# Performance work log

Hardware: AMD Instinct MI355X
Metric: run time of the kernel (lower is better)

The kernel has to match this reference:

```python
import jax, jax.numpy as jnp
import numpy as np

N_NODES = 100000
N_EDGES = 1600000
IN_DIM = 256
OUT_DIM = 128
SELF_LOOP_W = 2.0  # improved=True


def setup_inputs() -> dict:
    key = jax.random.key(0)
    ks = jax.random.split(key, 9)
    x = jax.random.normal(ks[0], (N_NODES, IN_DIM), dtype=jnp.float32)
    edge_index = jax.random.randint(ks[1], (2, N_EDGES), 0, N_NODES, dtype=jnp.int64)
    edge_weight = jax.random.uniform(ks[2], (N_EDGES,), dtype=jnp.float32)
    s1 = 1.0 / np.sqrt(IN_DIM)
    s2 = 1.0 / np.sqrt(OUT_DIM)
    W1 = jax.random.normal(ks[3], (IN_DIM, OUT_DIM), dtype=jnp.float32) * s1
    b1 = jnp.zeros((OUT_DIM,), dtype=jnp.float32)
    W_mu = jax.random.normal(ks[4], (OUT_DIM, OUT_DIM), dtype=jnp.float32) * s2
    b_mu = jnp.zeros((OUT_DIM,), dtype=jnp.float32)
    W_var = jax.random.normal(ks[5], (OUT_DIM, OUT_DIM), dtype=jnp.float32) * s2
    b_var = jnp.zeros((OUT_DIM,), dtype=jnp.float32)
    return {"x": x, "edge_index": edge_index, "edge_weight": edge_weight,
            "W1": W1, "b1": b1, "W_mu": W_mu, "b_mu": b_mu,
            "W_var": W_var, "b_var": b_var}


def _gcn_norm(edge_index, edge_weight, num_nodes):
    # add self loops with fill value 2.0 (improved=True), then symmetric norm
    loop = jnp.arange(num_nodes, dtype=edge_index.dtype)
    row = jnp.concatenate([edge_index[0], loop])
    col = jnp.concatenate([edge_index[1], loop])
    ew = jnp.concatenate([edge_weight,
                          jnp.full((num_nodes,), SELF_LOOP_W, dtype=edge_weight.dtype)])
    deg = jax.ops.segment_sum(ew, col, num_segments=num_nodes)
    dis = jnp.where(deg > 0, jax.lax.rsqrt(jnp.where(deg > 0, deg, 1.0)), 0.0)
    norm = dis[row] * ew * dis[col]
    return row, col, norm


def _gcn_conv(x, row, col, norm, W, b, num_nodes):
    xw = x @ W                      # [N, out]
    msg = xw[row] * norm[:, None]   # [E+N, out] per-edge messages
    out = jax.ops.segment_sum(msg, col, num_segments=num_nodes)
    return out + b


def reference(x, edge_index, edge_weight, W1, b1, W_mu, b_mu, W_var, b_var):
    n = x.shape[0]
    row, col, norm = _gcn_norm(edge_index, edge_weight, n)
    feat = jax.nn.relu(_gcn_conv(x, row, col, norm, W1, b1, n))
    mu = _gcn_conv(feat, row, col, norm, W_mu, b_mu, n)
    var = _gcn_conv(feat, row, col, norm, W_var, b_var, n)
    return (mu, var)
```

## Files before the change

kernel.cpp:

```cpp
#include <hip/hip_runtime.h>
#include <hip/hip_bf16.h>

#define CDIV(a,b) (((a)+(b)-1)/(b))

typedef __attribute__((ext_vector_type(8))) short short8;
typedef __attribute__((ext_vector_type(4))) float f32x4;

static __device__ inline short f2bf(float f) {
    union { __hip_bfloat16 h; short s; } u;
    u.h = __float2bfloat16(f);
    return u.s;
}
static __device__ inline ushort f2bfu(float f) { return (ushort)f2bf(f); }
static __device__ inline float bfu_lo(uint v) { return __uint_as_float(v << 16); }
static __device__ inline float bfu_hi(uint v) { return __uint_as_float(v & 0xffff0000u); }


__global__ __launch_bounds__(512) void k_init(const float* __restrict__ W1,
                                              short* __restrict__ W1t,
                                              const float* __restrict__ Wmu,
                                              const float* __restrict__ Wvar,
                                              short* __restrict__ Wcat) {
    int i = blockIdx.x * 512 + threadIdx.x;
    if (i < 128 * 256) {
        int k = i % 256, col = i / 256;
        W1t[i] = f2bf(W1[(size_t)k * 128 + col]);
    } else if (i < 2 * 128 * 256) {
        int j = i - 128 * 256;
        int k = j & 127, col = j >> 7;
        float v = (col < 128) ? Wmu[(size_t)k * 128 + col] : Wvar[(size_t)k * 128 + (col - 128)];
        Wcat[j] = f2bf(v);
    }
}


__global__ __launch_bounds__(512) void k_bhist(const int* __restrict__ coli,
                                               int* __restrict__ bhist,
                                               int E, int chunk, int nbk) {
    __shared__ int h[256];
    int b = blockIdx.x, t = threadIdx.x, nblk = gridDim.x;
    for (int i = t; i < nbk; i += 512) h[i] = 0;
    __syncthreads();
    int e0 = b * chunk, e1 = min(E, e0 + chunk);
    for (int e = e0 + t; e < e1; e += 512)
        atomicAdd(&h[coli[e] >> 9], 1);
    __syncthreads();
    for (int i = t; i < nbk; i += 512)
        bhist[i * nblk + b] = h[i];
}

__global__ __launch_bounds__(256) void kscanA(const int* __restrict__ in,
                                              int* __restrict__ out,
                                              int* __restrict__ part, int n) {
    int t = threadIdx.x;
    int base = blockIdx.x * 1024 + t * 4;
    int v0 = (base + 0 < n) ? in[base + 0] : 0;
    int v1 = (base + 1 < n) ? in[base + 1] : 0;
    int v2 = (base + 2 < n) ? in[base + 2] : 0;
    int v3 = (base + 3 < n) ? in[base + 3] : 0;
    int tsum = v0 + v1 + v2 + v3;
    int lane = t & 63, wv = t >> 6;
    int val = tsum;
    #pragma unroll
    for (int d = 1; d < 64; d <<= 1) {
        int u = __shfl_up(val, d, 64);
        if (lane >= d) val += u;
    }
    __shared__ int ws[4];
    if (lane == 63) ws[wv] = val;
    __syncthreads();
    int woff = 0;
    #pragma unroll
    for (int i = 0; i < 4; ++i) if (i < wv) woff += ws[i];
    int excl = woff + val - tsum;
    if (base + 0 < n) out[base + 0] = excl;  excl += v0;
    if (base + 1 < n) out[base + 1] = excl;  excl += v1;
    if (base + 2 < n) out[base + 2] = excl;  excl += v2;
    if (base + 3 < n) out[base + 3] = excl;
    if (t == 255) part[blockIdx.x] = woff + val;
}

__global__ __launch_bounds__(128) void kscanB(int* part, int nb, int* tailp, int tailv) {
    int t = threadIdx.x;
    int v = (t < nb) ? part[t] : 0;
    int lane = t & 63, wv = t >> 6;
    int val = v;
    #pragma unroll
    for (int d = 1; d < 64; d <<= 1) {
        int u = __shfl_up(val, d, 64);
        if (lane >= d) val += u;
    }
    __shared__ int ws[2];
    if (lane == 63) ws[wv] = val;
    __syncthreads();
    int woff = (wv == 1) ? ws[0] : 0;
    if (t < nb) part[t] = woff + val - v;
    if (t == 0 && tailp) *tailp = tailv;
}

__global__ __launch_bounds__(256) void kscanC(int* __restrict__ out,
                                              const int* __restrict__ part, int n) {
    int i = blockIdx.x * 256 + threadIdx.x;
    if (i < n) out[i] += part[i >> 10];
}

__global__ __launch_bounds__(512) void k_bucket(const int* __restrict__ rowi,
                                                const int* __restrict__ coli,
                                                const float* __restrict__ ew,
                                                const int* __restrict__ excl,
                                                int* __restrict__ bcol,
                                                int2* __restrict__ bre,
                                                int E, int chunk, int nbk) {
    __shared__ int cur[256];
    int b = blockIdx.x, t = threadIdx.x, nblk = gridDim.x;
    for (int i = t; i < nbk; i += 512) cur[i] = 0;
    __syncthreads();
    int e0 = b * chunk, e1 = min(E, e0 + chunk);
    for (int e = e0 + t; e < e1; e += 512) {
        int c = coli[e];
        int bk = c >> 9;
        int pos = excl[bk * nblk + b] + atomicAdd(&cur[bk], 1);
        bcol[pos] = c;
        bre[pos]  = make_int2(rowi[e], __float_as_int(ew[e]));
    }
}

__global__ __launch_bounds__(512) void k_fine(const int* __restrict__ bcol,
                                              const int2* __restrict__ bre,
                                              const int* __restrict__ excl,
                                              int* __restrict__ rank,
                                              int* __restrict__ gcnt,
                                              int* __restrict__ gews,
                                              int E, int nblk, int n) {
    __shared__ int cnt[512], ews[512];
    int bk = blockIdx.x, t = threadIdx.x;
    cnt[t] = 0; ews[t] = 0;
    __syncthreads();
    int s0 = excl[bk * nblk];
    int s1 = (bk + 1 < gridDim.x) ? excl[(bk + 1) * nblk] : E;
    for (int p = s0 + t; p < s1; p += 512) {
        int cl = bcol[p] & 511;
        rank[p] = atomicAdd(&cnt[cl], 1);
        int q = (int)(__int_as_float(bre[p].y) * 16777216.0f + 0.5f);
        atomicAdd(&ews[cl], q);
    }
    __syncthreads();
    int c = bk * 512 + t;
    if (c < n) { gcnt[c] = cnt[t]; gews[c] = ews[t]; }
}

__global__ __launch_bounds__(256) void k_dis(const int* __restrict__ gews,
                                             float* __restrict__ dis, int n) {
    int i = blockIdx.x * 256 + threadIdx.x;
    if (i < n)
        dis[i] = rsqrtf(2.0f + (float)gews[i] * (1.0f / 16777216.0f));
}

__global__ __launch_bounds__(512) void k_place(const int* __restrict__ bcol,
                                               const int2* __restrict__ bre,
                                               const int* __restrict__ rank,
                                               const int* __restrict__ row_ptr,
                                               const float* __restrict__ dis,
                                               int2* __restrict__ csr, int E) {
    int p = blockIdx.x * 512 + threadIdx.x;
    if (p < E) {
        int c = bcol[p];
        int2 re = bre[p];
        csr[row_ptr[c] + rank[p]] =
            make_int2(re.x, __float_as_int(dis[re.x] * __int_as_float(re.y)));
    }
}


__global__ __launch_bounds__(512) void k_gemm1(const float* __restrict__ A,
                                               const short* __restrict__ Bt,
                                               ushort* __restrict__ C, int n) {
    const int K = 256, KH = 128;
    __shared__ short Blds[128 * KH];
    int t = threadIdx.x;

    int wave = t >> 6, lane = t & 63;
    int lg = lane >> 4, lr = lane & 15;
    long row_base = (long)blockIdx.x * 256 + wave * 32;

    long ra0 = row_base + lr;      if (ra0 > n - 1) ra0 = n - 1;
    long ra1 = row_base + 16 + lr; if (ra1 > n - 1) ra1 = n - 1;

    f32x4 acc[2][8];
    #pragma unroll
    for (int i = 0; i < 2; ++i)
        #pragma unroll
        for (int j = 0; j < 8; ++j) acc[i][j] = (f32x4){0.f, 0.f, 0.f, 0.f};

    const float* pa0 = A + ra0 * K + lg * 8;
    const float* pa1 = A + ra1 * K + lg * 8;

    #pragma unroll
    for (int p = 0; p < 2; ++p) {
        if (p) __syncthreads();
        const int CHK = KH / 8;
        for (int c = t; c < 128 * CHK; c += 512) {
            int colw = c / CHK;
            int kb  = (c % CHK) * 16;
            int dst = colw * (KH * 2) + (kb ^ ((colw & 7) << 4));
            *(float4*)((char*)Blds + dst) =
                *(const float4*)((const char*)Bt + (size_t)colw * (K * 2) + p * (KH * 2) + kb);
        }
        __syncthreads();

        for (int k0 = 0; k0 < KH; k0 += 32) {
            int kg = p * KH + k0;
            float4 x0 = *(const float4*)(pa0 + kg);
            float4 x1 = *(const float4*)(pa0 + kg + 4);
            float4 y0 = *(const float4*)(pa1 + kg);
            float4 y1 = *(const float4*)(pa1 + kg + 4);
            short8 a0, a1;
            a0[0]=f2bf(x0.x); a0[1]=f2bf(x0.y); a0[2]=f2bf(x0.z); a0[3]=f2bf(x0.w);
            a0[4]=f2bf(x1.x); a0[5]=f2bf(x1.y); a0[6]=f2bf(x1.z); a0[7]=f2bf(x1.w);
            a1[0]=f2bf(y0.x); a1[1]=f2bf(y0.y); a1[2]=f2bf(y0.z); a1[3]=f2bf(y0.w);
            a1[4]=f2bf(y1.x); a1[5]=f2bf(y1.y); a1[6]=f2bf(y1.z); a1[7]=f2bf(y1.w);

            int kb = (k0 + lg * 8) * 2;
            #pragma unroll
            for (int cb = 0; cb < 8; ++cb) {
                int colm = cb * 16 + lr;
                short8 bfr = *(short8*)((char*)Blds + colm * (KH * 2) + (kb ^ ((colm & 7) << 4)));
                acc[0][cb] = __builtin_amdgcn_mfma_f32_16x16x32_bf16(a0, bfr, acc[0][cb], 0, 0, 0);
                acc[1][cb] = __builtin_amdgcn_mfma_f32_16x16x32_bf16(a1, bfr, acc[1][cb], 0, 0, 0);
            }
        }
    }

    #pragma unroll
    for (int rf = 0; rf < 2; ++rf) {
        #pragma unroll
        for (int cb = 0; cb < 8; ++cb) {
            int colm = cb * 16 + lr;
            #pragma unroll
            for (int r = 0; r < 4; ++r) {
                long row = row_base + rf * 16 + lg * 4 + r;
                if (row < n) C[row * 128 + colm] = f2bfu(acc[rf][cb][r]);
            }
        }
    }
}


template<int OUTMODE>
__global__ __launch_bounds__(256) void k_agg(const uint2* __restrict__ src,
                                             const int* __restrict__ row_ptr,
                                             const int2* __restrict__ csr,
                                             const float* __restrict__ dis,
                                             const float* __restrict__ bias,
                                             uint2* __restrict__ dst, int n) {
    int wid = (blockIdx.x * 256 + threadIdx.x) >> 6;
    int lane = threadIdx.x & 63;
    int hb = lane >> 5, lc = lane & 31;
    if (wid >= n) return;
    int e0 = row_ptr[wid], e1 = row_ptr[wid + 1];

    float p00=0.f,p01=0.f,p02=0.f,p03=0.f;
    float p10=0.f,p11=0.f,p12=0.f,p13=0.f;
    float p20=0.f,p21=0.f,p22=0.f,p23=0.f;
    float p30=0.f,p31=0.f,p32=0.f,p33=0.f;

    int e = e0;
    for (; e + 7 < e1; e += 8) {
        int2 c0 = csr[e     + hb];
        int2 c1 = csr[e + 2 + hb];
        int2 c2 = csr[e + 4 + hb];
        int2 c3 = csr[e + 6 + hb];
        uint2 v0 = src[(size_t)c0.x * 32 + lc];
        uint2 v1 = src[(size_t)c1.x * 32 + lc];
        uint2 v2 = src[(size_t)c2.x * 32 + lc];
        uint2 v3 = src[(size_t)c3.x * 32 + lc];
        float w0 = __int_as_float(c0.y), w1 = __int_as_float(c1.y);
        float w2 = __int_as_float(c2.y), w3 = __int_as_float(c3.y);
        p00 += w0 * bfu_lo(v0.x); p01 += w0 * bfu_hi(v0.x);
        p02 += w0 * bfu_lo(v0.y); p03 += w0 * bfu_hi(v0.y);
        p10 += w1 * bfu_lo(v1.x); p11 += w1 * bfu_hi(v1.x);
        p12 += w1 * bfu_lo(v1.y); p13 += w1 * bfu_hi(v1.y);
        p20 += w2 * bfu_lo(v2.x); p21 += w2 * bfu_hi(v2.x);
        p22 += w2 * bfu_lo(v2.y); p23 += w2 * bfu_hi(v2.y);
        p30 += w3 * bfu_lo(v3.x); p31 += w3 * bfu_hi(v3.x);
        p32 += w3 * bfu_lo(v3.y); p33 += w3 * bfu_hi(v3.y);
    }
    for (; e + 1 < e1; e += 2) {
        int2 c = csr[e + hb];
        uint2 v = src[(size_t)c.x * 32 + lc];
        float w = __int_as_float(c.y);
        p00 += w * bfu_lo(v.x); p01 += w * bfu_hi(v.x);
        p02 += w * bfu_lo(v.y); p03 += w * bfu_hi(v.y);
    }
    if (e < e1 && hb == 0) {
        int2 c = csr[e];
        uint2 v = src[(size_t)c.x * 32 + lc];
        float w = __int_as_float(c.y);
        p10 += w * bfu_lo(v.x); p11 += w * bfu_hi(v.x);
        p12 += w * bfu_lo(v.y); p13 += w * bfu_hi(v.y);
    }

    float x0 = (p00 + p10) + (p20 + p30);
    float x1 = (p01 + p11) + (p21 + p31);
    float x2 = (p02 + p12) + (p22 + p32);
    float x3 = (p03 + p13) + (p23 + p33);
    x0 = x0 + __shfl_xor(x0, 32);
    x1 = x1 + __shfl_xor(x1, 32);
    x2 = x2 + __shfl_xor(x2, 32);
    x3 = x3 + __shfl_xor(x3, 32);

    float dc = dis[wid];
    uint2 sv = src[(size_t)wid * 32 + lc];
    float sw = 2.f * dc * dc;
    float o0 = dc * x0 + sw * bfu_lo(sv.x);
    float o1 = dc * x1 + sw * bfu_hi(sv.x);
    float o2 = dc * x2 + sw * bfu_lo(sv.y);
    float o3 = dc * x3 + sw * bfu_hi(sv.y);
    if constexpr (OUTMODE == 0) {
        float4 bv = *(const float4*)(bias + lc * 4);
        o0 += bv.x; o1 += bv.y; o2 += bv.z; o3 += bv.w;
        o0 = fmaxf(o0, 0.f); o1 = fmaxf(o1, 0.f);
        o2 = fmaxf(o2, 0.f); o3 = fmaxf(o3, 0.f);
    }
    if (hb == 0)
        dst[(size_t)wid * 32 + lc] =
            make_uint2((uint)f2bfu(o0) | ((uint)f2bfu(o1) << 16),
                       (uint)f2bfu(o2) | ((uint)f2bfu(o3) << 16));
}


__global__ __launch_bounds__(512) void k_gemm2(const short* __restrict__ A,
                                               const short* __restrict__ Bt,
                                               const float* __restrict__ bmu,
                                               const float* __restrict__ bvar,
                                               float* __restrict__ out,
                                               int n) {
    const int K = 128;
    __shared__ short Blds[256 * K];
    int t = threadIdx.x;

    const int CHK = K / 8;
    for (int c = t; c < 256 * CHK; c += 512) {
        int col = c / CHK;
        int kb  = (c % CHK) * 16;
        int dst = col * (K * 2) + (kb ^ ((col & 7) << 4));
        *(float4*)((char*)Blds + dst) =
            *(const float4*)((const char*)Bt + (size_t)col * (K * 2) + kb);
    }
    __syncthreads();

    int wave = t >> 6, lane = t & 63;
    int lg = lane >> 4, lr = lane & 15;
    int colbase = (wave & 1) * 128;
    long row_base = (long)blockIdx.x * 128 + (wave >> 1) * 32;

    long ra0 = row_base + lr;      if (ra0 > n - 1) ra0 = n - 1;
    long ra1 = row_base + 16 + lr; if (ra1 > n - 1) ra1 = n - 1;

    f32x4 acc[2][8];
    #pragma unroll
    for (int i = 0; i < 2; ++i)
        #pragma unroll
        for (int j = 0; j < 8; ++j) acc[i][j] = (f32x4){0.f, 0.f, 0.f, 0.f};

    const short* pa0 = A + ra0 * K + lg * 8;
    const short* pa1 = A + ra1 * K + lg * 8;

    #pragma unroll
    for (int k0 = 0; k0 < K; k0 += 32) {
        short8 a0 = *(const short8*)(pa0 + k0);
        short8 a1 = *(const short8*)(pa1 + k0);
        int kb = (k0 + lg * 8) * 2;
        #pragma unroll
        for (int cb = 0; cb < 8; ++cb) {
            int col = colbase + cb * 16 + lr;
            short8 b = *(short8*)((char*)Blds + col * (K * 2) + (kb ^ ((col & 7) << 4)));
            acc[0][cb] = __builtin_amdgcn_mfma_f32_16x16x32_bf16(a0, b, acc[0][cb], 0, 0, 0);
            acc[1][cb] = __builtin_amdgcn_mfma_f32_16x16x32_bf16(a1, b, acc[1][cb], 0, 0, 0);
        }
    }

    #pragma unroll
    for (int rf = 0; rf < 2; ++rf) {
        #pragma unroll
        for (int cb = 0; cb < 8; ++cb) {
            int colc = colbase + cb * 16 + lr;
            bool is_var = colc >= 128;
            int col = is_var ? colc - 128 : colc;
            float bv = is_var ? bvar[col] : bmu[col];
            size_t obase = is_var ? (size_t)n * 128 : 0;
            #pragma unroll
            for (int r = 0; r < 4; ++r) {
                long row = row_base + rf * 16 + lg * 4 + r;
                if (row < n)
                    __builtin_nontemporal_store(acc[rf][cb][r] + bv,
                                                &out[obase + (size_t)row * 128 + col]);
            }
        }
    }
}


extern "C" void kernel_launch(void* const* d_in, const int* in_sizes, int n_in,
                              void* d_out, int out_size, void* d_ws, size_t ws_size,
                              hipStream_t stream) {
    const float* x    = (const float*)d_in[0];
    const int*   ei   = (const int*)d_in[1];
    const float* ew   = (const float*)d_in[2];
    const float* W1   = (const float*)d_in[3];
    const float* b1   = (const float*)d_in[4];
    const float* Wmu  = (const float*)d_in[5];
    const float* bmu  = (const float*)d_in[6];
    const float* Wvar = (const float*)d_in[7];
    const float* bvar = (const float*)d_in[8];

    const int E = in_sizes[2];
    const int N = in_sizes[0] / 256;
    const int* rowi = ei;
    const int* coli = ei + E;

    char* base = (char*)d_ws;
    size_t off = 0;
    auto alloc = [&](size_t bytes) -> void* {
        void* p = base + off;
        off = (off + bytes + 511) & ~(size_t)511;
        return p;
    };
    const int NBLK = 256;
    const int nbk  = CDIV(N, 512);
    const int chunk = CDIV(E, NBLK);
    const int nh   = nbk * NBLK;

    int*   bhist   = (int*)  alloc((size_t)nh * 4);
    int*   excl    = (int*)  alloc((size_t)nh * 4);
    int*   part    = (int*)  alloc(256 * 4);
    int*   bcol    = (int*)  alloc((size_t)E * 4);
    int2*  bre     = (int2*) alloc((size_t)E * 8);
    int*   rank    = (int*)  alloc((size_t)E * 4);
    int*   gcnt    = (int*)  alloc((size_t)N * 4);
    int*   gews    = (int*)  alloc((size_t)N * 4);
    int*   row_ptr = (int*)  alloc((size_t)(N + 1) * 4);
    float* dis     = (float*)alloc((size_t)N * 4);
    int2*  csr     = (int2*) alloc((size_t)E * 8);
    uint*  xw      = (uint*) alloc((size_t)N * 64 * 4);
    uint*  feat    = (uint*) alloc((size_t)N * 64 * 4);
    short* W1t     = (short*)alloc((size_t)256 * 128 * 2);
    short* Wcat    = (short*)alloc((size_t)256 * 128 * 2);
    uint*  g       = xw;

    k_init<<<CDIV(2 * 128 * 256, 512), 512, 0, stream>>>(W1, W1t, Wmu, Wvar, Wcat);

    k_gemm1<<<CDIV(N, 256), 512, 0, stream>>>(x, W1t, (ushort*)xw, N);

    k_bhist<<<NBLK, 512, 0, stream>>>(coli, bhist, E, chunk, nbk);
    kscanA<<<CDIV(nh, 1024), 256, 0, stream>>>(bhist, excl, part, nh);
    kscanB<<<1, 128, 0, stream>>>(part, CDIV(nh, 1024), nullptr, 0);
    kscanC<<<CDIV(nh, 256), 256, 0, stream>>>(excl, part, nh);
    k_bucket<<<NBLK, 512, 0, stream>>>(rowi, coli, ew, excl, bcol, bre, E, chunk, nbk);
    k_fine<<<nbk, 512, 0, stream>>>(bcol, bre, excl, rank, gcnt, gews, E, NBLK, N);
    kscanA<<<CDIV(N, 1024), 256, 0, stream>>>(gcnt, row_ptr, part, N);
    kscanB<<<1, 128, 0, stream>>>(part, CDIV(N, 1024), &row_ptr[N], E);
    kscanC<<<CDIV(N, 256), 256, 0, stream>>>(row_ptr, part, N);
    k_dis<<<CDIV(N, 256), 256, 0, stream>>>(gews, dis, N);
    k_place<<<CDIV(E, 512), 512, 0, stream>>>(bcol, bre, rank, row_ptr, dis, csr, E);

    k_agg<0><<<CDIV(N * 64, 256), 256, 0, stream>>>((const uint2*)xw, row_ptr, csr, dis, b1, (uint2*)feat, N);
    k_agg<1><<<CDIV(N * 64, 256), 256, 0, stream>>>((const uint2*)feat, row_ptr, csr, dis, nullptr, (uint2*)g, N);
    k_gemm2<<<CDIV(N, 128), 512, 0, stream>>>((const short*)g, Wcat, bmu, bvar, (float*)d_out, N);
}
```

Measured before the change: 286.6 us.

## Fuse CSR build: per-bucket local scan, packed bucket records, bucket-wise placement

```diff
diff --git a/kernel.cpp b/kernel.cpp
--- a/kernel.cpp
+++ b/kernel.cpp
@@ -80,7 +80,7 @@
     if (t == 255) part[blockIdx.x] = woff + val;
 }
 
-__global__ __launch_bounds__(128) void kscanB(int* part, int nb, int* tailp, int tailv) {
+__global__ __launch_bounds__(128) void kscanB(int* part, int nb) {
     int t = threadIdx.x;
     int v = (t < nb) ? part[t] : 0;
     int lane = t & 63, wv = t >> 6;
@@ -95,7 +95,6 @@
     __syncthreads();
     int woff = (wv == 1) ? ws[0] : 0;
     if (t < nb) part[t] = woff + val - v;
-    if (t == 0 && tailp) *tailp = tailv;
 }
 
 __global__ __launch_bounds__(256) void kscanC(int* __restrict__ out,
@@ -108,8 +107,8 @@
                                                 const int* __restrict__ coli,
                                                 const float* __restrict__ ew,
                                                 const int* __restrict__ excl,
-                                                int* __restrict__ bcol,
-                                                int2* __restrict__ bre,
+                                                int* __restrict__ bx,
+                                                int* __restrict__ bw,
                                                 int E, int chunk, int nbk) {
     __shared__ int cur[256];
     int b = blockIdx.x, t = threadIdx.x, nblk = gridDim.x;
@@ -120,18 +119,17 @@
         int c = coli[e];
         int bk = c >> 9;
         int pos = excl[bk * nblk + b] + atomicAdd(&cur[bk], 1);
-        bcol[pos] = c;
-        bre[pos]  = make_int2(rowi[e], __float_as_int(ew[e]));
-    }
-}
-
-__global__ __launch_bounds__(512) void k_fine(const int* __restrict__ bcol,
-                                              const int2* __restrict__ bre,
-                                              const int* __restrict__ excl,
-                                              int* __restrict__ rank,
-                                              int* __restrict__ gcnt,
-                                              int* __restrict__ gews,
-                                              int E, int nblk, int n) {
+        bx[pos] = ((c & 511) << 17) | rowi[e];
+        bw[pos] = __float_as_int(ew[e]);
+    }
+}
+
+__global__ __launch_bounds__(512) void k_fine2(const int* __restrict__ bx,
+                                               const int* __restrict__ bw,
+                                               const int* __restrict__ excl,
+                                               int* __restrict__ row_ptr,
+                                               float* __restrict__ dis,
+                                               int E, int nblk, int n) {
     __shared__ int cnt[512], ews[512];
     int bk = blockIdx.x, t = threadIdx.x;
     cnt[t] = 0; ews[t] = 0;
@@ -139,35 +137,54 @@
     int s0 = excl[bk * nblk];
     int s1 = (bk + 1 < gridDim.x) ? excl[(bk + 1) * nblk] : E;
     for (int p = s0 + t; p < s1; p += 512) {
-        int cl = bcol[p] & 511;
-        rank[p] = atomicAdd(&cnt[cl], 1);
-        int q = (int)(__int_as_float(bre[p].y) * 16777216.0f + 0.5f);
+        int cl = bx[p] >> 17;
+        atomicAdd(&cnt[cl], 1);
+        int q = (int)(__int_as_float(bw[p]) * 16777216.0f + 0.5f);
         atomicAdd(&ews[cl], q);
     }
     __syncthreads();
+    int v = cnt[t];
+    int lane = t & 63, wv = t >> 6;
+    int val = v;
+    #pragma unroll
+    for (int d = 1; d < 64; d <<= 1) {
+        int u = __shfl_up(val, d, 64);
+        if (lane >= d) val += u;
+    }
+    __shared__ int ws2[8];
+    if (lane == 63) ws2[wv] = val;
+    __syncthreads();
+    int woff = 0;
+    #pragma unroll
+    for (int i = 0; i < 8; ++i) if (i < wv) woff += ws2[i];
+    int lexcl = woff + val - v;
     int c = bk * 512 + t;
-    if (c < n) { gcnt[c] = cnt[t]; gews[c] = ews[t]; }
-}
-
-__global__ __launch_bounds__(256) void k_dis(const int* __restrict__ gews,
-                                             float* __restrict__ dis, int n) {
-    int i = blockIdx.x * 256 + threadIdx.x;
-    if (i < n)
-        dis[i] = rsqrtf(2.0f + (float)gews[i] * (1.0f / 16777216.0f));
-}
-
-__global__ __launch_bounds__(512) void k_place(const int* __restrict__ bcol,
-                                               const int2* __restrict__ bre,
-                                               const int* __restrict__ rank,
+    if (c < n) {
+        row_ptr[c] = s0 + lexcl;
+        dis[c] = rsqrtf(2.0f + (float)ews[t] * (1.0f / 16777216.0f));
+    }
+    if (bk == 0 && t == 0) row_ptr[n] = E;
+}
+
+__global__ __launch_bounds__(512) void k_place(const int* __restrict__ bx,
+                                               const int* __restrict__ bw,
+                                               const int* __restrict__ excl,
                                                const int* __restrict__ row_ptr,
                                                const float* __restrict__ dis,
-                                               int2* __restrict__ csr, int E) {
-    int p = blockIdx.x * 512 + threadIdx.x;
-    if (p < E) {
-        int c = bcol[p];
-        int2 re = bre[p];
-        csr[row_ptr[c] + rank[p]] =
-            make_int2(re.x, __float_as_int(dis[re.x] * __int_as_float(re.y)));
+                                               int2* __restrict__ csr,
+                                               int E, int nblk, int n) {
+    __shared__ int cur[512];
+    int bk = blockIdx.x, t = threadIdx.x;
+    cur[t] = 0;
+    __syncthreads();
+    int s0 = excl[bk * nblk];
+    int s1 = (bk + 1 < gridDim.x) ? excl[(bk + 1) * nblk] : E;
+    int cbase = bk * 512;
+    for (int p = s0 + t; p < s1; p += 512) {
+        int u = bx[p];
+        int cl = u >> 17, r = u & 0x1FFFF;
+        int pos = row_ptr[cbase + cl] + atomicAdd(&cur[cl], 1);
+        csr[pos] = make_int2(r, __float_as_int(dis[r] * __int_as_float(bw[p])));
     }
 }
 
@@ -265,11 +282,43 @@
     float p30=0.f,p31=0.f,p32=0.f,p33=0.f;
 
     int e = e0;
+    for (; e + 15 < e1; e += 16) {
+        int2 c0 = csr[e      + hb], c1 = csr[e + 2  + hb];
+        int2 c2 = csr[e + 4  + hb], c3 = csr[e + 6  + hb];
+        int2 c4 = csr[e + 8  + hb], c5 = csr[e + 10 + hb];
+        int2 c6 = csr[e + 12 + hb], c7 = csr[e + 14 + hb];
+        uint2 v0 = src[(size_t)c0.x * 32 + lc];
+        uint2 v1 = src[(size_t)c1.x * 32 + lc];
+        uint2 v2 = src[(size_t)c2.x * 32 + lc];
+        uint2 v3 = src[(size_t)c3.x * 32 + lc];
+        uint2 v4 = src[(size_t)c4.x * 32 + lc];
+        uint2 v5 = src[(size_t)c5.x * 32 + lc];
+        uint2 v6 = src[(size_t)c6.x * 32 + lc];
+        uint2 v7 = src[(size_t)c7.x * 32 + lc];
+        float w0 = __int_as_float(c0.y), w1 = __int_as_float(c1.y);
+        float w2 = __int_as_float(c2.y), w3 = __int_as_float(c3.y);
+        float w4 = __int_as_float(c4.y), w5 = __int_as_float(c5.y);
+        float w6 = __int_as_float(c6.y), w7 = __int_as_float(c7.y);
+        p00 += w0 * bfu_lo(v0.x); p01 += w0 * bfu_hi(v0.x);
+        p02 += w0 * bfu_lo(v0.y); p03 += w0 * bfu_hi(v0.y);
+        p10 += w1 * bfu_lo(v1.x); p11 += w1 * bfu_hi(v1.x);
+        p12 += w1 * bfu_lo(v1.y); p13 += w1 * bfu_hi(v1.y);
+        p20 += w2 * bfu_lo(v2.x); p21 += w2 * bfu_hi(v2.x);
+        p22 += w2 * bfu_lo(v2.y); p23 += w2 * bfu_hi(v2.y);
+        p30 += w3 * bfu_lo(v3.x); p31 += w3 * bfu_hi(v3.x);
+        p32 += w3 * bfu_lo(v3.y); p33 += w3 * bfu_hi(v3.y);
+        p00 += w4 * bfu_lo(v4.x); p01 += w4 * bfu_hi(v4.x);
+        p02 += w4 * bfu_lo(v4.y); p03 += w4 * bfu_hi(v4.y);
+        p10 += w5 * bfu_lo(v5.x); p11 += w5 * bfu_hi(v5.x);
+        p12 += w5 * bfu_lo(v5.y); p13 += w5 * bfu_hi(v5.y);
+        p20 += w6 * bfu_lo(v6.x); p21 += w6 * bfu_hi(v6.x);
+        p22 += w6 * bfu_lo(v6.y); p23 += w6 * bfu_hi(v6.y);
+        p30 += w7 * bfu_lo(v7.x); p31 += w7 * bfu_hi(v7.x);
+        p32 += w7 * bfu_lo(v7.y); p33 += w7 * bfu_hi(v7.y);
+    }
     for (; e + 7 < e1; e += 8) {
-        int2 c0 = csr[e     + hb];
-        int2 c1 = csr[e + 2 + hb];
-        int2 c2 = csr[e + 4 + hb];
-        int2 c3 = csr[e + 6 + hb];
+        int2 c0 = csr[e + hb],     c1 = csr[e + 2 + hb];
+        int2 c2 = csr[e + 4 + hb], c3 = csr[e + 6 + hb];
         uint2 v0 = src[(size_t)c0.x * 32 + lc];
         uint2 v1 = src[(size_t)c1.x * 32 + lc];
         uint2 v2 = src[(size_t)c2.x * 32 + lc];
@@ -434,11 +483,8 @@
     int*   bhist   = (int*)  alloc((size_t)nh * 4);
     int*   excl    = (int*)  alloc((size_t)nh * 4);
     int*   part    = (int*)  alloc(256 * 4);
-    int*   bcol    = (int*)  alloc((size_t)E * 4);
-    int2*  bre     = (int2*) alloc((size_t)E * 8);
-    int*   rank    = (int*)  alloc((size_t)E * 4);
-    int*   gcnt    = (int*)  alloc((size_t)N * 4);
-    int*   gews    = (int*)  alloc((size_t)N * 4);
+    int*   bx      = (int*)  alloc((size_t)E * 4);
+    int*   bw      = (int*)  alloc((size_t)E * 4);
     int*   row_ptr = (int*)  alloc((size_t)(N + 1) * 4);
     float* dis     = (float*)alloc((size_t)N * 4);
     int2*  csr     = (int2*) alloc((size_t)E * 8);
@@ -449,20 +495,15 @@
     uint*  g       = xw;
 
     k_init<<<CDIV(2 * 128 * 256, 512), 512, 0, stream>>>(W1, W1t, Wmu, Wvar, Wcat);
-
     k_gemm1<<<CDIV(N, 256), 512, 0, stream>>>(x, W1t, (ushort*)xw, N);
 
     k_bhist<<<NBLK, 512, 0, stream>>>(coli, bhist, E, chunk, nbk);
     kscanA<<<CDIV(nh, 1024), 256, 0, stream>>>(bhist, excl, part, nh);
-    kscanB<<<1, 128, 0, stream>>>(part, CDIV(nh, 1024), nullptr, 0);
+    kscanB<<<1, 128, 0, stream>>>(part, CDIV(nh, 1024));
     kscanC<<<CDIV(nh, 256), 256, 0, stream>>>(excl, part, nh);
-    k_bucket<<<NBLK, 512, 0, stream>>>(rowi, coli, ew, excl, bcol, bre, E, chunk, nbk);
-    k_fine<<<nbk, 512, 0, stream>>>(bcol, bre, excl, rank, gcnt, gews, E, NBLK, N);
-    kscanA<<<CDIV(N, 1024), 256, 0, stream>>>(gcnt, row_ptr, part, N);
-    kscanB<<<1, 128, 0, stream>>>(part, CDIV(N, 1024), &row_ptr[N], E);
-    kscanC<<<CDIV(N, 256), 256, 0, stream>>>(row_ptr, part, N);
-    k_dis<<<CDIV(N, 256), 256, 0, stream>>>(gews, dis, N);
-    k_place<<<CDIV(E, 512), 512, 0, stream>>>(bcol, bre, rank, row_ptr, dis, csr, E);
+    k_bucket<<<NBLK, 512, 0, stream>>>(rowi, coli, ew, excl, bx, bw, E, chunk, nbk);
+    k_fine2<<<nbk, 512, 0, stream>>>(bx, bw, excl, row_ptr, dis, E, NBLK, N);
+    k_place<<<nbk, 512, 0, stream>>>(bx, bw, excl, row_ptr, dis, csr, E, NBLK, N);
 
     k_agg<0><<<CDIV(N * 64, 256), 256, 0, stream>>>((const uint2*)xw, row_ptr, csr, dis, b1, (uint2*)feat, N);
     k_agg<1><<<CDIV(N * 64, 256), 256, 0, stream>>>((const uint2*)feat, row_ptr, csr, dis, nullptr, (uint2*)g, N);
```

Result: no change. 290.4 us (+1.4%).
